# Kernel tuning notes

Measured on AMD Instinct MI355X. Metric: run time of the kernel, lower is better.

The kernel has to match this reference:

```python
import jax, jax.numpy as jnp
import numpy as np

D_MODEL = 1024
N_HEADS = 16
D_V = D_MODEL // N_HEADS  # 64; o_proj maps d_model -> d_v (quirk of the source)
B, S = 4, 2048


def setup_inputs() -> dict:
    key = jax.random.key(0)
    ks = jax.random.split(key, 5)
    scale = 1.0 / np.sqrt(D_MODEL)
    return {
        "in_features": jax.random.normal(ks[0], (B, S, D_MODEL), dtype=jnp.float32),
        "Wq": jax.random.normal(ks[1], (D_MODEL, D_MODEL), dtype=jnp.float32) * scale,
        "Wk": jax.random.normal(ks[2], (D_MODEL, D_MODEL), dtype=jnp.float32) * scale,
        "Wv": jax.random.normal(ks[3], (D_MODEL, D_MODEL), dtype=jnp.float32) * scale,
        "Wo": jax.random.normal(ks[4], (D_V, D_MODEL), dtype=jnp.float32) * scale,
    }


def reference(in_features, Wq, Wk, Wv, Wo):
    # Linear(in, out): y = x @ W^T, no bias. NOTE: source never splits heads;
    # attention runs single-head over the full d_model dims.
    Q = jnp.einsum('bsd,ed->bse', in_features, Wq)  # [B,S,D]
    K = jnp.einsum('bsd,ed->bse', in_features, Wk)
    V = jnp.einsum('bsd,ed->bse', in_features, Wv)

    scores = jnp.einsum('bqd,bkd->bqk', Q, K)       # [B,S,S]
    causal = jnp.tril(jnp.ones((S, S), dtype=bool))  # True = keep
    # source applies -inf mask BEFORE scaling (equivalent result)
    scores = jnp.where(causal[None, :, :], scores, -jnp.inf)
    scores = scores / jnp.sqrt(jnp.float32(D_MODEL))  # K.size(-1) == d_model
    attn = jax.nn.softmax(scores, axis=-1)
    ctx = jnp.einsum('bqk,bkd->bqd', attn, V)        # [B,S,D]
    return jnp.einsum('bsd,vd->bsv', ctx, Wo)        # [B,S,D_V]
```

## Files before the change

kernel.cpp:

```cpp
#include <hip/hip_runtime.h>
#include <math.h>

typedef unsigned short u16;
typedef unsigned int u32;
typedef __attribute__((ext_vector_type(8))) short short8;
typedef __attribute__((ext_vector_type(4))) short short4v;
typedef __attribute__((ext_vector_type(4))) float f32x4;

#define BB 4
#define SS 2048
#define DD 1024
#define DV 64
#define NYU 1152
#define BS (BB * SS)
#define SCALE (1.0f / 32.0f)

__device__ __forceinline__ u16 f2bf(float f) {
    u32 u = __builtin_bit_cast(u32, f);
    u32 r = u + 0x7fffu + ((u >> 16) & 1u);
    return (u16)(r >> 16);
}
__device__ __forceinline__ float bf2f(u16 b) {
    return __builtin_bit_cast(float, (u32)b << 16);
}
__device__ __forceinline__ void storeC(float* p, float v) { *p = v; }
__device__ __forceinline__ void storeC(u16* p, float v) { *p = f2bf(v); }

__global__ __launch_bounds__(256) void prep(const float* __restrict__ x,
                                            const float* __restrict__ Wq,
                                            const float* __restrict__ Wk,
                                            const float* __restrict__ Wo,
                                            const float* __restrict__ Wv,
                                            u16* __restrict__ x16,
                                            u16* __restrict__ Wqt,
                                            u16* __restrict__ Wkt,
                                            float* __restrict__ wpart,
                                            float* __restrict__ out,
                                            float* __restrict__ Lacc) {
    __shared__ float smem[64 * 128];
    const int b = blockIdx.x;
    const int tid = threadIdx.x;
    if (b < 8192) {
        int i = b * 256 + tid;
        f32x4 v = ((const f32x4*)x)[i];
        short4v o;
        o.x = (short)f2bf(v.x); o.y = (short)f2bf(v.y);
        o.z = (short)f2bf(v.z); o.w = (short)f2bf(v.w);
        ((short4v*)x16)[i] = o;
    } else if (b < 8704) {
        const int bb = b - 8192;
        const float* src = (bb >> 8) ? Wk : Wq;
        u16* dst = (bb >> 8) ? Wkt : Wqt;
        const int rem = bb & 255;
        const int e0 = (rem >> 4) * 64, d0 = (rem & 15) * 64;
        u16* t = (u16*)smem;
        const int g = tid >> 6, lane = tid & 63;
        for (int r = g; r < 64; r += 4)
            t[r * 72 + lane] = f2bf(src[(size_t)(e0 + r) * DD + d0 + lane]);
        __syncthreads();
        for (int r = g; r < 64; r += 4)
            dst[(size_t)(d0 + r) * DD + e0 + lane] = t[lane * 72 + r];
    } else if (b < 8768) {
        const int bb = b - 8704;
        const int echunk = (bb & 7) * 128;
        const int kc = bb >> 3, kbase = kc * 128;
        for (int idx = tid; idx < 64 * 128; idx += 256)
            smem[idx] = Wo[(size_t)(idx >> 7) * DD + kbase + (idx & 127)];
        __syncthreads();
        const int eo = echunk + (tid & 31) * 4;
        const int ob = (tid >> 5) * 8;
        float acc[8][4] = {};
        for (int k = 0; k < 128; ++k) {
            f32x4 wv = *(const f32x4*)&Wv[(size_t)(kbase + k) * DD + eo];
#pragma unroll
            for (int oi = 0; oi < 8; ++oi) {
                float s = smem[(ob + oi) * 128 + k];
                acc[oi][0] += s * wv.x; acc[oi][1] += s * wv.y;
                acc[oi][2] += s * wv.z; acc[oi][3] += s * wv.w;
            }
        }
#pragma unroll
        for (int oi = 0; oi < 8; ++oi)
            *(f32x4*)&wpart[((size_t)kc * 64 + ob + oi) * DD + eo] =
                (f32x4){acc[oi][0], acc[oi][1], acc[oi][2], acc[oi][3]};
    } else if (b < 9280) {
        int i = (b - 8768) * 256 + tid;
        ((f32x4*)out)[i] = (f32x4){0.f, 0.f, 0.f, 0.f};
    } else {
        int i = (b - 9280) * 256 + tid;
        ((f32x4*)Lacc)[i] = (f32x4){0.f, 0.f, 0.f, 0.f};
    }
}

__global__ __launch_bounds__(256) void reduce_all(const float* __restrict__ Gpart,
                                                  const float* __restrict__ wpart,
                                                  u16* __restrict__ Wall2) {
    const int bx = blockIdx.x;
    const int e0 = threadIdx.x * 4;
    f32x4 s = (f32x4){0.f, 0.f, 0.f, 0.f};
    if (bx < 1024) {
#pragma unroll
        for (int kc = 0; kc < 4; ++kc)
            s += *(const f32x4*)&Gpart[(size_t)kc * DD * DD + (size_t)bx * DD + e0];
    } else {
#pragma unroll
        for (int kc = 0; kc < 8; ++kc)
            s += *(const f32x4*)&wpart[((size_t)kc * 64 + bx - 1024) * DD + e0];
    }
    short4v ov;
    ov.x = (short)f2bf(s.x); ov.y = (short)f2bf(s.y);
    ov.z = (short)f2bf(s.z); ov.w = (short)f2bf(s.w);
    *(short4v*)&Wall2[(size_t)bx * DD + e0] = ov;
}

template <int TM, int TN, int WM, int WN, typename OutT, int MODE>
__global__ __launch_bounds__(WM * WN * 64) void gemm_nt_mfma(
    const u16* __restrict__ A, const u16* __restrict__ B, OutT* __restrict__ C,
    int lda, int ldb, int ldc, int K, long sA, long sB, long sC,
    u16* __restrict__ Utp) {
    constexpr int NW = WM * WN;
    constexpr int CA = TM / 16;
    constexpr int CB = TN / 16;

    const int z = blockIdx.z;
    A += (size_t)z * sA;
    B += (size_t)z * sB;
    C += (size_t)z * sC;
    int m0, n0;
    if constexpr (MODE == 3) {
        const int b = blockIdx.x;
        const int r = b & 7, q = b >> 3;
        m0 = (r * 8 + q / 9) * TM;
        n0 = (q % 9) * TN;
    } else {
        m0 = blockIdx.y * TM;
        n0 = blockIdx.x * TN;
    }

    __shared__ u16 As[TM * 32];
    __shared__ u16 Bs[TN * 32];

    const int tid = threadIdx.x;
    const int w = tid >> 6, lane = tid & 63;
    const int wm = w / WN, wn = w % WN;
    const int lrow = lane >> 2;
    const int lcol = (lane & 3) * 8;
    const int m16 = lane & 15;
    const int kh = (lane >> 4) * 8;

    f32x4 acc[4][4];
#pragma unroll
    for (int i = 0; i < 4; ++i)
#pragma unroll
        for (int j = 0; j < 4; ++j) acc[i][j] = (f32x4){0.f, 0.f, 0.f, 0.f};

    for (int k0 = 0; k0 < K; k0 += 32) {
        for (int c = w; c < CA; c += NW) {
            const u16* g = A + (size_t)(m0 + c * 16 + lrow) * lda + k0 + lcol;
            __builtin_amdgcn_global_load_lds(
                (const __attribute__((address_space(1))) void*)g,
                (__attribute__((address_space(3))) void*)(&As[c * 512]), 16, 0, 0);
        }
        for (int c = w; c < CB; c += NW) {
            const u16* g = B + (size_t)(n0 + c * 16 + lrow) * ldb + k0 + lcol;
            __builtin_amdgcn_global_load_lds(
                (const __attribute__((address_space(1))) void*)g,
                (__attribute__((address_space(3))) void*)(&Bs[c * 512]), 16, 0, 0);
        }
        __syncthreads();

        short8 a[4], b[4];
#pragma unroll
        for (int i = 0; i < 4; ++i)
            a[i] = *(const short8*)&As[(wm * 64 + i * 16 + m16) * 32 + kh];
#pragma unroll
        for (int j = 0; j < 4; ++j)
            b[j] = *(const short8*)&Bs[(wn * 64 + j * 16 + m16) * 32 + kh];
#pragma unroll
        for (int i = 0; i < 4; ++i)
#pragma unroll
            for (int j = 0; j < 4; ++j)
                acc[i][j] = __builtin_amdgcn_mfma_f32_16x16x32_bf16(a[i], b[j], acc[i][j], 0, 0, 0);
        __syncthreads();
    }

    const int crow0 = m0 + wm * 64 + (lane >> 4) * 4;
    const int ccol0 = n0 + wn * 64 + m16;
#pragma unroll
    for (int i = 0; i < 4; ++i)
#pragma unroll
        for (int j = 0; j < 4; ++j)
#pragma unroll
            for (int r = 0; r < 4; ++r) {
                const float v = acc[i][j][r];
                storeC(&C[(size_t)(crow0 + i * 16 + r) * ldc + ccol0 + j * 16], v);
                if constexpr (MODE == 3) {
                    if (n0 == 1024 && wn == 0)
                        Utp[(size_t)(ccol0 + j * 16 - 1024) * BS + crow0 + i * 16 + r] = f2bf(v);
                }
            }
}

__global__ __launch_bounds__(256) void scores_pv(const u16* __restrict__ YU,
                                                 const u16* __restrict__ x16,
                                                 const u16* __restrict__ Ut,
                                                 float* __restrict__ out,
                                                 float* __restrict__ Lacc) {
    const int b = blockIdx.x;
    const int r8 = b & 7;
    const int z = r8 >> 1;
    const int t = 2 * (b >> 3) + (r8 & 1);
    int y = (int)((sqrtf(8.f * t + 1.f) - 1.f) * 0.5f);
    while ((y + 1) * (y + 2) / 2 <= t) ++y;
    while (y * (y + 1) / 2 > t) --y;
    const int m0 = y * 128;
    const int n0 = (t - y * (y + 1) / 2) * 128;

    const u16* A = YU + (size_t)z * SS * NYU;
    const u16* B = x16 + (size_t)z * SS * DD;

    __shared__ union ShU {
        struct { u16 As[128 * 32]; u16 Bs[128 * 32]; } s;
        u16 Ps[128 * 136];
    } sh;

    const int tid = threadIdx.x;
    const int w = tid >> 6, lane = tid & 63;
    const int wm = w >> 1, wn = w & 1;
    const int lrow = lane >> 2;
    const int lcol = (lane & 3) * 8;
    const int m16 = lane & 15;
    const int kh = (lane >> 4) * 8;

    f32x4 acc[4][4];
#pragma unroll
    for (int i = 0; i < 4; ++i)
#pragma unroll
        for (int j = 0; j < 4; ++j) acc[i][j] = (f32x4){0.f, 0.f, 0.f, 0.f};

    for (int k0 = 0; k0 < DD; k0 += 32) {
        for (int c = w; c < 8; c += 4) {
            const u16* g = A + (size_t)(m0 + c * 16 + lrow) * NYU + k0 + lcol;
            __builtin_amdgcn_global_load_lds(
                (const __attribute__((address_space(1))) void*)g,
                (__attribute__((address_space(3))) void*)(&sh.s.As[c * 512]), 16, 0, 0);
        }
        for (int c = w; c < 8; c += 4) {
            const u16* g = B + (size_t)(n0 + c * 16 + lrow) * DD + k0 + lcol;
            __builtin_amdgcn_global_load_lds(
                (const __attribute__((address_space(1))) void*)g,
                (__attribute__((address_space(3))) void*)(&sh.s.Bs[c * 512]), 16, 0, 0);
        }
        __syncthreads();

        short8 a[4], bb[4];
#pragma unroll
        for (int i = 0; i < 4; ++i)
            a[i] = *(const short8*)&sh.s.As[(wm * 64 + i * 16 + m16) * 32 + kh];
#pragma unroll
        for (int j = 0; j < 4; ++j)
            bb[j] = *(const short8*)&sh.s.Bs[(wn * 64 + j * 16 + m16) * 32 + kh];
#pragma unroll
        for (int i = 0; i < 4; ++i)
#pragma unroll
            for (int j = 0; j < 4; ++j)
                acc[i][j] = __builtin_amdgcn_mfma_f32_16x16x32_bf16(a[i], bb[j], acc[i][j], 0, 0, 0);
        __syncthreads();
    }

    const int rl0 = wm * 64 + (lane >> 4) * 4;
    const int cl0 = wn * 64 + m16;
#pragma unroll
    for (int i = 0; i < 4; ++i)
#pragma unroll
        for (int j = 0; j < 4; ++j)
#pragma unroll
            for (int r = 0; r < 4; ++r) {
                const int rl = rl0 + i * 16 + r;
                const int cl = cl0 + j * 16;
                float p = __expf(acc[i][j][r] * SCALE);
                sh.Ps[rl * 136 + cl] = (n0 + cl <= m0 + rl) ? f2bf(p) : (u16)0;
            }
    __syncthreads();

    short8 ones8;
#pragma unroll
    for (int e = 0; e < 8; ++e) ones8[e] = (short)0x3F80;

    const u16* Utz = Ut + (size_t)z * SS + n0;
    f32x4 accO[2][4], accL[2];
#pragma unroll
    for (int i = 0; i < 2; ++i) {
        accL[i] = (f32x4){0.f, 0.f, 0.f, 0.f};
#pragma unroll
        for (int j = 0; j < 4; ++j) accO[i][j] = (f32x4){0.f, 0.f, 0.f, 0.f};
    }
#pragma unroll
    for (int ks = 0; ks < 4; ++ks) {
        const int k0 = ks * 32;
        short8 a[2], bb[4];
#pragma unroll
        for (int i = 0; i < 2; ++i)
            a[i] = *(const short8*)&sh.Ps[(w * 32 + i * 16 + m16) * 136 + k0 + kh];
#pragma unroll
        for (int j = 0; j < 4; ++j)
            bb[j] = *(const short8*)&Utz[(size_t)(j * 16 + m16) * BS + k0 + kh];
#pragma unroll
        for (int i = 0; i < 2; ++i) {
#pragma unroll
            for (int j = 0; j < 4; ++j)
                accO[i][j] = __builtin_amdgcn_mfma_f32_16x16x32_bf16(a[i], bb[j], accO[i][j], 0, 0, 0);
            accL[i] = __builtin_amdgcn_mfma_f32_16x16x32_bf16(a[i], ones8, accL[i], 0, 0, 0);
        }
    }

    float* Oz = out + (size_t)z * SS * DV;
    float* Lz = Lacc + (size_t)z * SS;
    const int wrow = m0 + w * 32 + (lane >> 4) * 4;
#pragma unroll
    for (int i = 0; i < 2; ++i) {
#pragma unroll
        for (int j = 0; j < 4; ++j)
#pragma unroll
            for (int r = 0; r < 4; ++r)
                atomicAdd(&Oz[(size_t)(wrow + i * 16 + r) * DV + j * 16 + m16],
                          accO[i][j][r]);
        if (m16 == 0)
#pragma unroll
            for (int r = 0; r < 4; ++r)
                atomicAdd(&Lz[wrow + i * 16 + r], accL[i][r]);
    }
}

__global__ __launch_bounds__(256) void normalize(float* __restrict__ out,
                                                 const float* __restrict__ Lacc) {
    int i = blockIdx.x * 256 + threadIdx.x;
    f32x4 v = ((f32x4*)out)[i];
    const float inv = 1.f / Lacc[(i * 4) >> 6];
    v.x *= inv; v.y *= inv; v.z *= inv; v.w *= inv;
    ((f32x4*)out)[i] = v;
}

extern "C" void kernel_launch(void* const* d_in, const int* in_sizes, int n_in,
                              void* d_out, int out_size, void* d_ws, size_t ws_size,
                              hipStream_t stream) {
    const float* x  = (const float*)d_in[0];
    const float* Wq = (const float*)d_in[1];
    const float* Wk = (const float*)d_in[2];
    const float* Wv = (const float*)d_in[3];
    const float* Wo = (const float*)d_in[4];
    float* out = (float*)d_out;

    u16* x16   = (u16*)d_ws;
    u16* Wqt16 = x16 + (size_t)BB * SS * DD;
    u16* Wkt16 = Wqt16 + (size_t)DD * DD;
    u16* Wall2 = Wkt16 + (size_t)DD * DD;
    u16* YU    = Wall2 + (size_t)NYU * DD;
    u16* Ut    = YU + (size_t)BB * SS * NYU;
    float* wpart = (float*)(Ut + (size_t)DV * BS);
    float* Lacc  = wpart + (size_t)8 * 64 * DD;
    float* Gpart = (float*)YU;

    prep<<<dim3(9288), 256, 0, stream>>>(x, Wq, Wk, Wo, Wv, x16, Wqt16, Wkt16,
                                         wpart, out, Lacc);

    gemm_nt_mfma<128, 128, 2, 2, float, 0><<<dim3(8, 8, 4), 256, 0, stream>>>(
        Wkt16, Wqt16, Gpart, DD, DD, DD, 256, 256, 256, (long)DD * DD, nullptr);

    reduce_all<<<dim3(1088), 256, 0, stream>>>(Gpart, wpart, Wall2);

    gemm_nt_mfma<128, 128, 2, 2, u16, 3><<<dim3(576), 256, 0, stream>>>(
        x16, Wall2, YU, DD, DD, NYU, DD, 0, 0, 0, Ut);

    scores_pv<<<dim3(544), 256, 0, stream>>>(YU, x16, Ut, out, Lacc);

    normalize<<<dim3(out_size / 4 / 256), 256, 0, stream>>>(out, Lacc);
}
```

Before: 204.4 us.

## Fuse all pipeline stages into one cooperative persistent kernel with grid syncs

Replaces the six separate kernel launches (prep, Gram GEMM, reduce, projection GEMM, scores+PV, normalize) with a single cooperative kernel of 512 persistent blocks. The blocks loop over the work units of each stage and separate stages with grid.sync(). The aim is to remove per-launch overhead and inter-kernel gaps. The cost is grid barrier latency, fewer resident blocks in stages that had more parallelism, and a shared-memory union that raises LDS use across every stage. If the cooperative launch fails, the code falls back to the original multi-kernel path.

```diff
diff --git a/kernel.cpp b/kernel.cpp
--- a/kernel.cpp
+++ b/kernel.cpp
@@ -1,5 +1,8 @@
 #include <hip/hip_runtime.h>
+#include <hip/hip_cooperative_groups.h>
 #include <math.h>
+
+namespace cg = cooperative_groups;
 
 typedef unsigned short u16;
 typedef unsigned int u32;
@@ -14,29 +17,356 @@
 #define NYU 1152
 #define BS (BB * SS)
 #define SCALE (1.0f / 32.0f)
+#define NB 512
 
 __device__ __forceinline__ u16 f2bf(float f) {
     u32 u = __builtin_bit_cast(u32, f);
     u32 r = u + 0x7fffu + ((u >> 16) & 1u);
     return (u16)(r >> 16);
 }
-__device__ __forceinline__ float bf2f(u16 b) {
-    return __builtin_bit_cast(float, (u32)b << 16);
-}
-__device__ __forceinline__ void storeC(float* p, float v) { *p = v; }
-__device__ __forceinline__ void storeC(u16* p, float v) { *p = f2bf(v); }
-
-__global__ __launch_bounds__(256) void prep(const float* __restrict__ x,
-                                            const float* __restrict__ Wq,
-                                            const float* __restrict__ Wk,
-                                            const float* __restrict__ Wo,
-                                            const float* __restrict__ Wv,
-                                            u16* __restrict__ x16,
-                                            u16* __restrict__ Wqt,
-                                            u16* __restrict__ Wkt,
-                                            float* __restrict__ wpart,
-                                            float* __restrict__ out,
-                                            float* __restrict__ Lacc) {
+
+__global__ __launch_bounds__(256, 2) void mega(
+    const float* __restrict__ x, const float* __restrict__ Wq,
+    const float* __restrict__ Wk, const float* __restrict__ Wv,
+    const float* __restrict__ Wo,
+    u16* __restrict__ x16, u16* __restrict__ Wqt, u16* __restrict__ Wkt,
+    u16* __restrict__ Wall2, u16* __restrict__ YU, u16* __restrict__ Ut,
+    float* __restrict__ Gpart, float* __restrict__ wpart,
+    float* __restrict__ Lacc, float* __restrict__ out) {
+    cg::grid_group grid = cg::this_grid();
+
+    __shared__ union Sh {
+        float fbuf[64 * 128];
+        struct { u16 As[128 * 32]; u16 Bs[128 * 32]; } s;
+        u16 Ps[128 * 136];
+    } sh;
+
+    const int tid = threadIdx.x;
+    const int w = tid >> 6, lane = tid & 63;
+    const int wm = w >> 1, wn = w & 1;
+    const int lrow = lane >> 2;
+    const int lcol = (lane & 3) * 8;
+    const int m16 = lane & 15;
+    const int kh = (lane >> 4) * 8;
+    const int q4 = (lane >> 4) * 4;
+
+    for (int u = blockIdx.x; u < 9288; u += NB) {
+        if (u < 64) {
+            __syncthreads();
+            const int echunk = (u & 7) * 128;
+            const int kc = u >> 3, kbase = kc * 128;
+            for (int idx = tid; idx < 64 * 128; idx += 256)
+                sh.fbuf[idx] = Wo[(size_t)(idx >> 7) * DD + kbase + (idx & 127)];
+            __syncthreads();
+            const int eo = echunk + (tid & 31) * 4;
+            const int ob = (tid >> 5) * 8;
+            float acc[8][4] = {};
+            for (int k = 0; k < 128; ++k) {
+                f32x4 wv = *(const f32x4*)&Wv[(size_t)(kbase + k) * DD + eo];
+#pragma unroll
+                for (int oi = 0; oi < 8; ++oi) {
+                    float s = sh.fbuf[(ob + oi) * 128 + k];
+                    acc[oi][0] += s * wv.x; acc[oi][1] += s * wv.y;
+                    acc[oi][2] += s * wv.z; acc[oi][3] += s * wv.w;
+                }
+            }
+#pragma unroll
+            for (int oi = 0; oi < 8; ++oi)
+                *(f32x4*)&wpart[((size_t)kc * 64 + ob + oi) * DD + eo] =
+                    (f32x4){acc[oi][0], acc[oi][1], acc[oi][2], acc[oi][3]};
+            __syncthreads();
+        } else if (u < 576) {
+            __syncthreads();
+            const int bb = u - 64;
+            const float* src = (bb >> 8) ? Wk : Wq;
+            u16* dst = (bb >> 8) ? Wkt : Wqt;
+            const int rem = bb & 255;
+            const int e0 = (rem >> 4) * 64, d0 = (rem & 15) * 64;
+            u16* t = (u16*)sh.fbuf;
+            for (int r = w; r < 64; r += 4)
+                t[r * 72 + lane] = f2bf(src[(size_t)(e0 + r) * DD + d0 + lane]);
+            __syncthreads();
+            for (int r = w; r < 64; r += 4)
+                dst[(size_t)(d0 + r) * DD + e0 + lane] = t[lane * 72 + r];
+            __syncthreads();
+        } else if (u < 8768) {
+            int i = (u - 576) * 256 + tid;
+            f32x4 v = ((const f32x4*)x)[i];
+            short4v o;
+            o.x = (short)f2bf(v.x); o.y = (short)f2bf(v.y);
+            o.z = (short)f2bf(v.z); o.w = (short)f2bf(v.w);
+            ((short4v*)x16)[i] = o;
+        } else if (u < 9280) {
+            int i = (u - 8768) * 256 + tid;
+            ((f32x4*)out)[i] = (f32x4){0.f, 0.f, 0.f, 0.f};
+        } else {
+            int i = (u - 9280) * 256 + tid;
+            ((f32x4*)Lacc)[i] = (f32x4){0.f, 0.f, 0.f, 0.f};
+        }
+    }
+    grid.sync();
+
+    for (int u = blockIdx.x; u < 256; u += NB) {
+        const int xg = u & 7, yg = (u >> 3) & 7, zg = u >> 6;
+        const int m0 = yg * 128, n0 = xg * 128, kbase = zg * 256;
+        float* C = Gpart + (size_t)zg * DD * DD;
+
+        f32x4 acc[4][4];
+#pragma unroll
+        for (int i = 0; i < 4; ++i)
+#pragma unroll
+            for (int j = 0; j < 4; ++j) acc[i][j] = (f32x4){0.f, 0.f, 0.f, 0.f};
+
+        for (int k0 = 0; k0 < 256; k0 += 32) {
+            for (int c = w; c < 8; c += 4) {
+                const u16* g = Wkt + (size_t)(m0 + c * 16 + lrow) * DD + kbase + k0 + lcol;
+                __builtin_amdgcn_global_load_lds(
+                    (const __attribute__((address_space(1))) void*)g,
+                    (__attribute__((address_space(3))) void*)(&sh.s.As[c * 512]), 16, 0, 0);
+            }
+            for (int c = w; c < 8; c += 4) {
+                const u16* g = Wqt + (size_t)(n0 + c * 16 + lrow) * DD + kbase + k0 + lcol;
+                __builtin_amdgcn_global_load_lds(
+                    (const __attribute__((address_space(1))) void*)g,
+                    (__attribute__((address_space(3))) void*)(&sh.s.Bs[c * 512]), 16, 0, 0);
+            }
+            __syncthreads();
+            short8 a[4], b[4];
+#pragma unroll
+            for (int i = 0; i < 4; ++i)
+                a[i] = *(const short8*)&sh.s.As[(wm * 64 + i * 16 + m16) * 32 + kh];
+#pragma unroll
+            for (int j = 0; j < 4; ++j)
+                b[j] = *(const short8*)&sh.s.Bs[(wn * 64 + j * 16 + m16) * 32 + kh];
+#pragma unroll
+            for (int i = 0; i < 4; ++i)
+#pragma unroll
+                for (int j = 0; j < 4; ++j)
+                    acc[i][j] = __builtin_amdgcn_mfma_f32_16x16x32_bf16(a[i], b[j], acc[i][j], 0, 0, 0);
+            __syncthreads();
+        }
+        const int crow0 = m0 + wm * 64 + q4;
+        const int ccol0 = n0 + wn * 64 + m16;
+#pragma unroll
+        for (int i = 0; i < 4; ++i)
+#pragma unroll
+            for (int j = 0; j < 4; ++j)
+#pragma unroll
+                for (int r = 0; r < 4; ++r)
+                    C[(size_t)(crow0 + i * 16 + r) * DD + ccol0 + j * 16] = acc[i][j][r];
+    }
+    grid.sync();
+
+    for (int u = blockIdx.x; u < 1088; u += NB) {
+        const int e0 = tid * 4;
+        f32x4 s = (f32x4){0.f, 0.f, 0.f, 0.f};
+        if (u < 1024) {
+#pragma unroll
+            for (int kc = 0; kc < 4; ++kc)
+                s += *(const f32x4*)&Gpart[(size_t)kc * DD * DD + (size_t)u * DD + e0];
+        } else {
+#pragma unroll
+            for (int kc = 0; kc < 8; ++kc)
+                s += *(const f32x4*)&wpart[((size_t)kc * 64 + u - 1024) * DD + e0];
+        }
+        short4v ov;
+        ov.x = (short)f2bf(s.x); ov.y = (short)f2bf(s.y);
+        ov.z = (short)f2bf(s.z); ov.w = (short)f2bf(s.w);
+        *(short4v*)&Wall2[(size_t)u * DD + e0] = ov;
+    }
+    grid.sync();
+
+    for (int u = blockIdx.x; u < 576; u += NB) {
+        const int r = u & 7, q = u >> 3;
+        const int m0 = (r * 8 + q / 9) * 128;
+        const int n0 = (q % 9) * 128;
+
+        f32x4 acc[4][4];
+#pragma unroll
+        for (int i = 0; i < 4; ++i)
+#pragma unroll
+            for (int j = 0; j < 4; ++j) acc[i][j] = (f32x4){0.f, 0.f, 0.f, 0.f};
+
+        for (int k0 = 0; k0 < DD; k0 += 32) {
+            for (int c = w; c < 8; c += 4) {
+                const u16* g = x16 + (size_t)(m0 + c * 16 + lrow) * DD + k0 + lcol;
+                __builtin_amdgcn_global_load_lds(
+                    (const __attribute__((address_space(1))) void*)g,
+                    (__attribute__((address_space(3))) void*)(&sh.s.As[c * 512]), 16, 0, 0);
+            }
+            for (int c = w; c < 8; c += 4) {
+                const u16* g = Wall2 + (size_t)(n0 + c * 16 + lrow) * DD + k0 + lcol;
+                __builtin_amdgcn_global_load_lds(
+                    (const __attribute__((address_space(1))) void*)g,
+                    (__attribute__((address_space(3))) void*)(&sh.s.Bs[c * 512]), 16, 0, 0);
+            }
+            __syncthreads();
+            short8 a[4], b[4];
+#pragma unroll
+            for (int i = 0; i < 4; ++i)
+                a[i] = *(const short8*)&sh.s.As[(wm * 64 + i * 16 + m16) * 32 + kh];
+#pragma unroll
+            for (int j = 0; j < 4; ++j)
+                b[j] = *(const short8*)&sh.s.Bs[(wn * 64 + j * 16 + m16) * 32 + kh];
+#pragma unroll
+            for (int i = 0; i < 4; ++i)
+#pragma unroll
+                for (int j = 0; j < 4; ++j)
+                    acc[i][j] = __builtin_amdgcn_mfma_f32_16x16x32_bf16(a[i], b[j], acc[i][j], 0, 0, 0);
+            __syncthreads();
+        }
+        const int crow0 = m0 + wm * 64 + q4;
+        const int ccol0 = n0 + wn * 64 + m16;
+#pragma unroll
+        for (int i = 0; i < 4; ++i)
+#pragma unroll
+            for (int j = 0; j < 4; ++j)
+#pragma unroll
+                for (int r2 = 0; r2 < 4; ++r2) {
+                    const float v = acc[i][j][r2];
+                    const int row = crow0 + i * 16 + r2;
+                    const int col = ccol0 + j * 16;
+                    YU[(size_t)row * NYU + col] = f2bf(v);
+                    if (n0 == 1024 && wn == 0)
+                        Ut[(size_t)(col - 1024) * BS + row] = f2bf(v);
+                }
+    }
+    grid.sync();
+
+    for (int u = blockIdx.x; u < 544; u += NB) {
+        __syncthreads();
+        const int r8 = u & 7;
+        const int z = r8 >> 1;
+        const int t = 2 * (u >> 3) + (r8 & 1);
+        int y = (int)((sqrtf(8.f * t + 1.f) - 1.f) * 0.5f);
+        while ((y + 1) * (y + 2) / 2 <= t) ++y;
+        while (y * (y + 1) / 2 > t) --y;
+        const int m0 = y * 128;
+        const int n0 = (t - y * (y + 1) / 2) * 128;
+
+        const u16* A = YU + (size_t)z * SS * NYU;
+        const u16* B = x16 + (size_t)z * SS * DD;
+
+        f32x4 acc[4][4];
+#pragma unroll
+        for (int i = 0; i < 4; ++i)
+#pragma unroll
+            for (int j = 0; j < 4; ++j) acc[i][j] = (f32x4){0.f, 0.f, 0.f, 0.f};
+
+        for (int k0 = 0; k0 < DD; k0 += 32) {
+            for (int c = w; c < 8; c += 4) {
+                const u16* g = A + (size_t)(m0 + c * 16 + lrow) * NYU + k0 + lcol;
+                __builtin_amdgcn_global_load_lds(
+                    (const __attribute__((address_space(1))) void*)g,
+                    (__attribute__((address_space(3))) void*)(&sh.s.As[c * 512]), 16, 0, 0);
+            }
+            for (int c = w; c < 8; c += 4) {
+                const u16* g = B + (size_t)(n0 + c * 16 + lrow) * DD + k0 + lcol;
+                __builtin_amdgcn_global_load_lds(
+                    (const __attribute__((address_space(1))) void*)g,
+                    (__attribute__((address_space(3))) void*)(&sh.s.Bs[c * 512]), 16, 0, 0);
+            }
+            __syncthreads();
+            short8 a[4], bb[4];
+#pragma unroll
+            for (int i = 0; i < 4; ++i)
+                a[i] = *(const short8*)&sh.s.As[(wm * 64 + i * 16 + m16) * 32 + kh];
+#pragma unroll
+            for (int j = 0; j < 4; ++j)
+                bb[j] = *(const short8*)&sh.s.Bs[(wn * 64 + j * 16 + m16) * 32 + kh];
+#pragma unroll
+            for (int i = 0; i < 4; ++i)
+#pragma unroll
+                for (int j = 0; j < 4; ++j)
+                    acc[i][j] = __builtin_amdgcn_mfma_f32_16x16x32_bf16(a[i], bb[j], acc[i][j], 0, 0, 0);
+            __syncthreads();
+        }
+
+        const int rl0 = wm * 64 + q4;
+        const int cl0 = wn * 64 + m16;
+#pragma unroll
+        for (int i = 0; i < 4; ++i)
+#pragma unroll
+            for (int j = 0; j < 4; ++j)
+#pragma unroll
+                for (int r2 = 0; r2 < 4; ++r2) {
+                    const int rl = rl0 + i * 16 + r2;
+                    const int cl = cl0 + j * 16;
+                    float p = __expf(acc[i][j][r2] * SCALE);
+                    sh.Ps[rl * 136 + cl] = (n0 + cl <= m0 + rl) ? f2bf(p) : (u16)0;
+                }
+        __syncthreads();
+
+        short8 ones8;
+#pragma unroll
+        for (int e = 0; e < 8; ++e) ones8[e] = (short)0x3F80;
+
+        const u16* Utz = Ut + (size_t)z * SS + n0;
+        f32x4 accO[2][4], accL[2];
+#pragma unroll
+        for (int i = 0; i < 2; ++i) {
+            accL[i] = (f32x4){0.f, 0.f, 0.f, 0.f};
+#pragma unroll
+            for (int j = 0; j < 4; ++j) accO[i][j] = (f32x4){0.f, 0.f, 0.f, 0.f};
+        }
+#pragma unroll
+        for (int ks = 0; ks < 4; ++ks) {
+            const int k0 = ks * 32;
+            short8 a[2], bb[4];
+#pragma unroll
+            for (int i = 0; i < 2; ++i)
+                a[i] = *(const short8*)&sh.Ps[(w * 32 + i * 16 + m16) * 136 + k0 + kh];
+#pragma unroll
+            for (int j = 0; j < 4; ++j)
+                bb[j] = *(const short8*)&Utz[(size_t)(j * 16 + m16) * BS + k0 + kh];
+#pragma unroll
+            for (int i = 0; i < 2; ++i) {
+#pragma unroll
+                for (int j = 0; j < 4; ++j)
+                    accO[i][j] = __builtin_amdgcn_mfma_f32_16x16x32_bf16(a[i], bb[j], accO[i][j], 0, 0, 0);
+                accL[i] = __builtin_amdgcn_mfma_f32_16x16x32_bf16(a[i], ones8, accL[i], 0, 0, 0);
+            }
+        }
+
+        float* Oz = out + (size_t)z * SS * DV;
+        float* Lz = Lacc + (size_t)z * SS;
+        const int wrow = m0 + w * 32 + q4;
+#pragma unroll
+        for (int i = 0; i < 2; ++i) {
+#pragma unroll
+            for (int j = 0; j < 4; ++j)
+#pragma unroll
+                for (int r2 = 0; r2 < 4; ++r2)
+                    atomicAdd(&Oz[(size_t)(wrow + i * 16 + r2) * DV + j * 16 + m16],
+                              accO[i][j][r2]);
+            if (m16 == 0)
+#pragma unroll
+                for (int r2 = 0; r2 < 4; ++r2)
+                    atomicAdd(&Lz[wrow + i * 16 + r2], accL[i][r2]);
+        }
+    }
+    grid.sync();
+
+    for (int u = blockIdx.x; u < 512; u += NB) {
+        int i = u * 256 + tid;
+        f32x4 v = ((f32x4*)out)[i];
+        const float inv = 1.f / Lacc[(i * 4) >> 6];
+        v.x *= inv; v.y *= inv; v.z *= inv; v.w *= inv;
+        ((f32x4*)out)[i] = v;
+    }
+}
+
+__global__ __launch_bounds__(256) void prep_k(const float* __restrict__ x,
+                                              const float* __restrict__ Wq,
+                                              const float* __restrict__ Wk,
+                                              const float* __restrict__ Wo,
+                                              const float* __restrict__ Wv,
+                                              u16* __restrict__ x16,
+                                              u16* __restrict__ Wqt,
+                                              u16* __restrict__ Wkt,
+                                              float* __restrict__ wpart,
+                                              float* __restrict__ out,
+                                              float* __restrict__ Lacc) {
     __shared__ float smem[64 * 128];
     const int b = blockIdx.x;
     const int tid = threadIdx.x;
@@ -92,9 +422,66 @@
     }
 }
 
-__global__ __launch_bounds__(256) void reduce_all(const float* __restrict__ Gpart,
-                                                  const float* __restrict__ wpart,
-                                                  u16* __restrict__ Wall2) {
+__global__ __launch_bounds__(256) void gt_k(const u16* __restrict__ A,
+                                            const u16* __restrict__ B,
+                                            float* __restrict__ C0) {
+    const int zg = blockIdx.z;
+    const int m0 = blockIdx.y * 128, n0 = blockIdx.x * 128, kbase = zg * 256;
+    float* C = C0 + (size_t)zg * DD * DD;
+    __shared__ u16 As[128 * 32];
+    __shared__ u16 Bs[128 * 32];
+    const int tid = threadIdx.x;
+    const int w = tid >> 6, lane = tid & 63;
+    const int wm = w >> 1, wn = w & 1;
+    const int lrow = lane >> 2, lcol = (lane & 3) * 8;
+    const int m16 = lane & 15, kh = (lane >> 4) * 8;
+    f32x4 acc[4][4];
+#pragma unroll
+    for (int i = 0; i < 4; ++i)
+#pragma unroll
+        for (int j = 0; j < 4; ++j) acc[i][j] = (f32x4){0.f, 0.f, 0.f, 0.f};
+    for (int k0 = 0; k0 < 256; k0 += 32) {
+        for (int c = w; c < 8; c += 4) {
+            const u16* g = A + (size_t)(m0 + c * 16 + lrow) * DD + kbase + k0 + lcol;
+            __builtin_amdgcn_global_load_lds(
+                (const __attribute__((address_space(1))) void*)g,
+                (__attribute__((address_space(3))) void*)(&As[c * 512]), 16, 0, 0);
+        }
+        for (int c = w; c < 8; c += 4) {
+            const u16* g = B + (size_t)(n0 + c * 16 + lrow) * DD + kbase + k0 + lcol;
+            __builtin_amdgcn_global_load_lds(
+                (const __attribute__((address_space(1))) void*)g,
+                (__attribute__((address_space(3))) void*)(&Bs[c * 512]), 16, 0, 0);
+        }
+        __syncthreads();
+        short8 a[4], b[4];
+#pragma unroll
+        for (int i = 0; i < 4; ++i)
+            a[i] = *(const short8*)&As[(wm * 64 + i * 16 + m16) * 32 + kh];
+#pragma unroll
+        for (int j = 0; j < 4; ++j)
+            b[j] = *(const short8*)&Bs[(wn * 64 + j * 16 + m16) * 32 + kh];
+#pragma unroll
+        for (int i = 0; i < 4; ++i)
+#pragma unroll
+            for (int j = 0; j < 4; ++j)
+                acc[i][j] = __builtin_amdgcn_mfma_f32_16x16x32_bf16(a[i], b[j], acc[i][j], 0, 0, 0);
+        __syncthreads();
+    }
+    const int crow0 = m0 + wm * 64 + (lane >> 4) * 4;
+    const int ccol0 = n0 + wn * 64 + m16;
+#pragma unroll
+    for (int i = 0; i < 4; ++i)
+#pragma unroll
+        for (int j = 0; j < 4; ++j)
+#pragma unroll
+            for (int r = 0; r < 4; ++r)
+                C[(size_t)(crow0 + i * 16 + r) * DD + ccol0 + j * 16] = acc[i][j][r];
+}
+
+__global__ __launch_bounds__(256) void reduce_k(const float* __restrict__ Gpart,
+                                                const float* __restrict__ wpart,
+                                                u16* __restrict__ Wall2) {
     const int bx = blockIdx.x;
     const int e0 = threadIdx.x * 4;
     f32x4 s = (f32x4){0.f, 0.f, 0.f, 0.f};
@@ -113,77 +500,54 @@
     *(short4v*)&Wall2[(size_t)bx * DD + e0] = ov;
 }
 
-template <int TM, int TN, int WM, int WN, typename OutT, int MODE>
-__global__ __launch_bounds__(WM * WN * 64) void gemm_nt_mfma(
-    const u16* __restrict__ A, const u16* __restrict__ B, OutT* __restrict__ C,
-    int lda, int ldb, int ldc, int K, long sA, long sB, long sC,
-    u16* __restrict__ Utp) {
-    constexpr int NW = WM * WN;
-    constexpr int CA = TM / 16;
-    constexpr int CB = TN / 16;
-
-    const int z = blockIdx.z;
-    A += (size_t)z * sA;
-    B += (size_t)z * sB;
-    C += (size_t)z * sC;
-    int m0, n0;
-    if constexpr (MODE == 3) {
-        const int b = blockIdx.x;
-        const int r = b & 7, q = b >> 3;
-        m0 = (r * 8 + q / 9) * TM;
-        n0 = (q % 9) * TN;
-    } else {
-        m0 = blockIdx.y * TM;
-        n0 = blockIdx.x * TN;
-    }
-
-    __shared__ u16 As[TM * 32];
-    __shared__ u16 Bs[TN * 32];
-
+__global__ __launch_bounds__(256) void yu_k(const u16* __restrict__ A,
+                                            const u16* __restrict__ B,
+                                            u16* __restrict__ C,
+                                            u16* __restrict__ Utp) {
+    const int b = blockIdx.x;
+    const int r = b & 7, q = b >> 3;
+    const int m0 = (r * 8 + q / 9) * 128;
+    const int n0 = (q % 9) * 128;
+    __shared__ u16 As[128 * 32];
+    __shared__ u16 Bs[128 * 32];
     const int tid = threadIdx.x;
     const int w = tid >> 6, lane = tid & 63;
-    const int wm = w / WN, wn = w % WN;
-    const int lrow = lane >> 2;
-    const int lcol = (lane & 3) * 8;
-    const int m16 = lane & 15;
-    const int kh = (lane >> 4) * 8;
-
+    const int wm = w >> 1, wn = w & 1;
+    const int lrow = lane >> 2, lcol = (lane & 3) * 8;
+    const int m16 = lane & 15, kh = (lane >> 4) * 8;
     f32x4 acc[4][4];
 #pragma unroll
     for (int i = 0; i < 4; ++i)
 #pragma unroll
         for (int j = 0; j < 4; ++j) acc[i][j] = (f32x4){0.f, 0.f, 0.f, 0.f};
-
-    for (int k0 = 0; k0 < K; k0 += 32) {
-        for (int c = w; c < CA; c += NW) {
-            const u16* g = A + (size_t)(m0 + c * 16 + lrow) * lda + k0 + lcol;
+    for (int k0 = 0; k0 < DD; k0 += 32) {
+        for (int c = w; c < 8; c += 4) {
+            const u16* g = A + (size_t)(m0 + c * 16 + lrow) * DD + k0 + lcol;
             __builtin_amdgcn_global_load_lds(
                 (const __attribute__((address_space(1))) void*)g,
                 (__attribute__((address_space(3))) void*)(&As[c * 512]), 16, 0, 0);
         }
-        for (int c = w; c < CB; c += NW) {
-            const u16* g = B + (size_t)(n0 + c * 16 + lrow) * ldb + k0 + lcol;
+        for (int c = w; c < 8; c += 4) {
+            const u16* g = B + (size_t)(n0 + c * 16 + lrow) * DD + k0 + lcol;
             __builtin_amdgcn_global_load_lds(
                 (const __attribute__((address_space(1))) void*)g,
                 (__attribute__((address_space(3))) void*)(&Bs[c * 512]), 16, 0, 0);
         }
         __syncthreads();
-
-        short8 a[4], b[4];
+        short8 a[4], bb[4];
 #pragma unroll
         for (int i = 0; i < 4; ++i)
             a[i] = *(const short8*)&As[(wm * 64 + i * 16 + m16) * 32 + kh];
 #pragma unroll
         for (int j = 0; j < 4; ++j)
-            b[j] = *(const short8*)&Bs[(wn * 64 + j * 16 + m16) * 32 + kh];
-#pragma unroll
-        for (int i = 0; i < 4; ++i)
-#pragma unroll
-            for (int j = 0; j < 4; ++j)
-                acc[i][j] = __builtin_amdgcn_mfma_f32_16x16x32_bf16(a[i], b[j], acc[i][j], 0, 0, 0);
-        __syncthreads();
-    }
-
+            bb[j] = *(const short8*)&Bs[(wn * 64 + j * 16 + m16) * 32 + kh];
+#pragma unroll
+        for (int i = 0; i < 4; ++i)
+#pragma unroll
+            for (int j = 0; j < 4; ++j)
+                acc[i][j] = __builtin_amdgcn_mfma_f32_16x16x32_bf16(a[i], bb[j], acc[i][j], 0, 0, 0);
+        __syncthreads();
+    }
     const int crow0 = m0 + wm * 64 + (lane >> 4) * 4;
     const int ccol0 = n0 + wn * 64 + m16;
 #pragma unroll
@@ -191,21 +555,21 @@
 #pragma unroll
         for (int j = 0; j < 4; ++j)
 #pragma unroll
-            for (int r = 0; r < 4; ++r) {
-                const float v = acc[i][j][r];
-                storeC(&C[(size_t)(crow0 + i * 16 + r) * ldc + ccol0 + j * 16], v);
-                if constexpr (MODE == 3) {
-                    if (n0 == 1024 && wn == 0)
-                        Utp[(size_t)(ccol0 + j * 16 - 1024) * BS + crow0 + i * 16 + r] = f2bf(v);
-                }
-            }
-}
-
-__global__ __launch_bounds__(256) void scores_pv(const u16* __restrict__ YU,
-                                                 const u16* __restrict__ x16,
-                                                 const u16* __restrict__ Ut,
-                                                 float* __restrict__ out,
-                                                 float* __restrict__ Lacc) {
+            for (int r2 = 0; r2 < 4; ++r2) {
+                const float v = acc[i][j][r2];
+                const int row = crow0 + i * 16 + r2;
+                const int col = ccol0 + j * 16;
+                C[(size_t)row * NYU + col] = f2bf(v);
+                if (n0 == 1024 && wn == 0)
+                    Utp[(size_t)(col - 1024) * BS + row] = f2bf(v);
+            }
+}
+
+__global__ __launch_bounds__(256) void spv_k(const u16* __restrict__ YU,
+                                             const u16* __restrict__ x16,
+                                             const u16* __restrict__ Ut,
+                                             float* __restrict__ out,
+                                             float* __restrict__ Lacc) {
     const int b = blockIdx.x;
     const int r8 = b & 7;
     const int z = r8 >> 1;
@@ -215,29 +579,22 @@
     while (y * (y + 1) / 2 > t) --y;
     const int m0 = y * 128;
     const int n0 = (t - y * (y + 1) / 2) * 128;
-
     const u16* A = YU + (size_t)z * SS * NYU;
     const u16* B = x16 + (size_t)z * SS * DD;
-
     __shared__ union ShU {
         struct { u16 As[128 * 32]; u16 Bs[128 * 32]; } s;
         u16 Ps[128 * 136];
     } sh;
-
     const int tid = threadIdx.x;
     const int w = tid >> 6, lane = tid & 63;
     const int wm = w >> 1, wn = w & 1;
-    const int lrow = lane >> 2;
-    const int lcol = (lane & 3) * 8;
-    const int m16 = lane & 15;
-    const int kh = (lane >> 4) * 8;
-
+    const int lrow = lane >> 2, lcol = (lane & 3) * 8;
+    const int m16 = lane & 15, kh = (lane >> 4) * 8;
     f32x4 acc[4][4];
 #pragma unroll
     for (int i = 0; i < 4; ++i)
 #pragma unroll
         for (int j = 0; j < 4; ++j) acc[i][j] = (f32x4){0.f, 0.f, 0.f, 0.f};
-
     for (int k0 = 0; k0 < DD; k0 += 32) {
         for (int c = w; c < 8; c += 4) {
             const u16* g = A + (size_t)(m0 + c * 16 + lrow) * NYU + k0 + lcol;
@@ -252,7 +609,6 @@
                 (__attribute__((address_space(3))) void*)(&sh.s.Bs[c * 512]), 16, 0, 0);
         }
         __syncthreads();
-
         short8 a[4], bb[4];
 #pragma unroll
         for (int i = 0; i < 4; ++i)
@@ -267,7 +623,6 @@
                 acc[i][j] = __builtin_amdgcn_mfma_f32_16x16x32_bf16(a[i], bb[j], acc[i][j], 0, 0, 0);
         __syncthreads();
     }
-
     const int rl0 = wm * 64 + (lane >> 4) * 4;
     const int cl0 = wn * 64 + m16;
 #pragma unroll
@@ -275,18 +630,16 @@
 #pragma unroll
         for (int j = 0; j < 4; ++j)
 #pragma unroll
-            for (int r = 0; r < 4; ++r) {
-                const int rl = rl0 + i * 16 + r;
+            for (int r2 = 0; r2 < 4; ++r2) {
+                const int rl = rl0 + i * 16 + r2;
                 const int cl = cl0 + j * 16;
-                float p = __expf(acc[i][j][r] * SCALE);
+                float p = __expf(acc[i][j][r2] * SCALE);
                 sh.Ps[rl * 136 + cl] = (n0 + cl <= m0 + rl) ? f2bf(p) : (u16)0;
             }
     __syncthreads();
-
     short8 ones8;
 #pragma unroll
     for (int e = 0; e < 8; ++e) ones8[e] = (short)0x3F80;
-
     const u16* Utz = Ut + (size_t)z * SS + n0;
     f32x4 accO[2][4], accL[2];
 #pragma unroll
@@ -313,7 +666,6 @@
             accL[i] = __builtin_amdgcn_mfma_f32_16x16x32_bf16(a[i], ones8, accL[i], 0, 0, 0);
         }
     }
-
     float* Oz = out + (size_t)z * SS * DV;
     float* Lz = Lacc + (size_t)z * SS;
     const int wrow = m0 + w * 32 + (lane >> 4) * 4;
@@ -322,18 +674,18 @@
 #pragma unroll
         for (int j = 0; j < 4; ++j)
 #pragma unroll
-            for (int r = 0; r < 4; ++r)
-                atomicAdd(&Oz[(size_t)(wrow + i * 16 + r) * DV + j * 16 + m16],
-                          accO[i][j][r]);
+            for (int r2 = 0; r2 < 4; ++r2)
+                atomicAdd(&Oz[(size_t)(wrow + i * 16 + r2) * DV + j * 16 + m16],
+                          accO[i][j][r2]);
         if (m16 == 0)
 #pragma unroll
-            for (int r = 0; r < 4; ++r)
-                atomicAdd(&Lz[wrow + i * 16 + r], accL[i][r]);
-    }
-}
-
-__global__ __launch_bounds__(256) void normalize(float* __restrict__ out,
-                                                 const float* __restrict__ Lacc) {
+            for (int r2 = 0; r2 < 4; ++r2)
+                atomicAdd(&Lz[wrow + i * 16 + r2], accL[i][r2]);
+    }
+}
+
+__global__ __launch_bounds__(256) void norm_k(float* __restrict__ out,
+                                              const float* __restrict__ Lacc) {
     int i = blockIdx.x * 256 + threadIdx.x;
     f32x4 v = ((f32x4*)out)[i];
     const float inv = 1.f / Lacc[(i * 4) >> 6];
@@ -361,18 +713,19 @@
     float* Lacc  = wpart + (size_t)8 * 64 * DD;
     float* Gpart = (float*)YU;
 
-    prep<<<dim3(9288), 256, 0, stream>>>(x, Wq, Wk, Wo, Wv, x16, Wqt16, Wkt16,
-                                         wpart, out, Lacc);
-
-    gemm_nt_mfma<128, 128, 2, 2, float, 0><<<dim3(8, 8, 4), 256, 0, stream>>>(
-        Wkt16, Wqt16, Gpart, DD, DD, DD, 256, 256, 256, (long)DD * DD, nullptr);
-
-    reduce_all<<<dim3(1088), 256, 0, stream>>>(Gpart, wpart, Wall2);
-
-    gemm_nt_mfma<128, 128, 2, 2, u16, 3><<<dim3(576), 256, 0, stream>>>(
-        x16, Wall2, YU, DD, DD, NYU, DD, 0, 0, 0, Ut);
-
-    scores_pv<<<dim3(544), 256, 0, stream>>>(YU, x16, Ut, out, Lacc);
-
-    normalize<<<dim3(out_size / 4 / 256), 256, 0, stream>>>(out, Lacc);
-}
+    void* args[] = {(void*)&x, (void*)&Wq, (void*)&Wk, (void*)&Wv, (void*)&Wo,
+                    (void*)&x16, (void*)&Wqt16, (void*)&Wkt16, (void*)&Wall2,
+                    (void*)&YU, (void*)&Ut, (void*)&Gpart, (void*)&wpart,
+                    (void*)&Lacc, (void*)&out};
+    hipError_t err = hipLaunchCooperativeKernel((const void*)mega, dim3(NB),
+                                                dim3(256), args, 0, stream);
+    if (err != hipSuccess) {
+        prep_k<<<dim3(9288), 256, 0, stream>>>(x, Wq, Wk, Wo, Wv, x16, Wqt16,
+                                               Wkt16, wpart, out, Lacc);
+        gt_k<<<dim3(8, 8, 4), 256, 0, stream>>>(Wkt16, Wqt16, Gpart);
+        reduce_k<<<dim3(1088), 256, 0, stream>>>(Gpart, wpart, Wall2);
+        yu_k<<<dim3(576), 256, 0, stream>>>(x16, Wall2, YU, Ut);
+        spv_k<<<dim3(544), 256, 0, stream>>>(YU, x16, Ut, out, Lacc);
+        norm_k<<<dim3(BS * DV / 4 / 256), 256, 0, stream>>>(out, Lacc);
+    }
+}
```

Measured after the change: 677.8 us. +231.5%, slower.
